# Kernel tuning notes

Measured on AMD Instinct MI355X. Metric: run time of the kernel, lower is better.

## Reference

```python
import jax, jax.numpy as jnp
import numpy as np

OUT_F, IN_F, GS = 11008, 4096, 64        # out_features, in_features, group_size
TOKENS = 4096
G = OUT_F * IN_F // GS                    # number of quantization groups = 704512


def setup_inputs() -> dict:
    key = jax.random.key(0)
    k1, k2, k3, k4, k5 = jax.random.split(key, 5)
    x = jax.random.normal(k1, (TOKENS, IN_F), dtype=jnp.float32)
    # packed 4-bit weights: two 4-bit values per byte (high nibble = first half rows)
    W_q = jax.random.randint(k2, (GS // 2, G), 0, 256, dtype=jnp.int32)
    # per-group dequant params: scale = 1/s (small positive), zero in [0, 15]
    scale = jax.random.uniform(k3, (1, G), dtype=jnp.float32, minval=1e-3, maxval=1e-2)
    zero = jax.random.uniform(k4, (1, G), dtype=jnp.float32, minval=0.0, maxval=15.0)
    bias = jax.random.normal(k5, (OUT_F,), dtype=jnp.float32) * 0.01
    return {"x": x, "W_q": W_q, "scale": scale, "zero": zero, "bias": bias}


def _dequantize(W_q, scale, zero):
    # BitPack.unpack_4bit_u8: first half of rows from high nibble, second half from low nibble
    hi = ((W_q >> 4) & 0xF).astype(jnp.float32)   # [GS//2, G]
    lo = (W_q & 0xF).astype(jnp.float32)          # [GS//2, G]
    W_r = jnp.concatenate([hi, lo], axis=0)       # [GS, G]
    # (W_r - zero) * scale, then reshape back to the original weight shape
    return ((W_r - zero) * scale).reshape(OUT_F, IN_F)


def reference(x, W_q, scale, zero, bias):
    # HQQMatmulNoCacheDeq.forward: out = x @ dequantize().T + bias
    W = _dequantize(W_q, scale, zero)             # [OUT_F, IN_F]
    return x @ W.T + bias                         # [TOKENS, OUT_F]
```

## Files before the change

kernel.cpp:

```cpp
#include <hip/hip_runtime.h>

#define TOK  4096
#define INF  4096
#define OUTF 11008
#define NG   704512
#define QD   172

typedef __bf16 bf16x8 __attribute__((ext_vector_type(8)));
typedef float  floatx4 __attribute__((ext_vector_type(4)));

__device__ inline void glds16(const __bf16* g, __bf16* l) {
  __builtin_amdgcn_global_load_lds(
      (const __attribute__((address_space(1))) void*)g,
      (__attribute__((address_space(3))) void*)l,
      16, 0, 0);
}

__global__ __launch_bounds__(256) void convert_x_kernel(
    const float* __restrict__ x, __bf16* __restrict__ Xb) {
  size_t i = ((size_t)blockIdx.x * 256 + threadIdx.x) * 8;
  float4 a = *(const float4*)(x + i);
  float4 b = *(const float4*)(x + i + 4);
  bf16x8 o;
  o[0] = (__bf16)a.x; o[1] = (__bf16)a.y; o[2] = (__bf16)a.z; o[3] = (__bf16)a.w;
  o[4] = (__bf16)b.x; o[5] = (__bf16)b.y; o[6] = (__bf16)b.z; o[7] = (__bf16)b.w;
  *(bf16x8*)(Xb + i) = o;
}

__global__ __launch_bounds__(256) void dequant_w_kernel(
    const int* __restrict__ Wq, const float* __restrict__ sc,
    const float* __restrict__ zp, __bf16* __restrict__ Wb) {
  const int b = blockIdx.x;
  const int r = b / QD;
  const int q = b - r * QD;
  const int*   wrow = Wq + (size_t)r * NG + (size_t)q * INF;
  const float* srow = sc + (size_t)q * INF;
  const float* zrow = zp + (size_t)q * INF;
  __bf16* hrow = Wb + (size_t)(r * QD + q) * INF;
  __bf16* lrow = Wb + (size_t)((r + 32) * QD + q) * INF;
#pragma unroll
  for (int it = 0; it < 2; ++it) {
    const int k = ((int)threadIdx.x + it * 256) * 8;
    int4   w0 = *(const int4*)(wrow + k);
    int4   w1 = *(const int4*)(wrow + k + 4);
    float4 s0 = *(const float4*)(srow + k);
    float4 s1 = *(const float4*)(srow + k + 4);
    float4 z0 = *(const float4*)(zrow + k);
    float4 z1 = *(const float4*)(zrow + k + 4);
    bf16x8 hi, lo;
    hi[0] = (__bf16)(((float)((w0.x >> 4) & 0xF) - z0.x) * s0.x);
    hi[1] = (__bf16)(((float)((w0.y >> 4) & 0xF) - z0.y) * s0.y);
    hi[2] = (__bf16)(((float)((w0.z >> 4) & 0xF) - z0.z) * s0.z);
    hi[3] = (__bf16)(((float)((w0.w >> 4) & 0xF) - z0.w) * s0.w);
    hi[4] = (__bf16)(((float)((w1.x >> 4) & 0xF) - z1.x) * s1.x);
    hi[5] = (__bf16)(((float)((w1.y >> 4) & 0xF) - z1.y) * s1.y);
    hi[6] = (__bf16)(((float)((w1.z >> 4) & 0xF) - z1.z) * s1.z);
    hi[7] = (__bf16)(((float)((w1.w >> 4) & 0xF) - z1.w) * s1.w);
    lo[0] = (__bf16)(((float)(w0.x & 0xF) - z0.x) * s0.x);
    lo[1] = (__bf16)(((float)(w0.y & 0xF) - z0.y) * s0.y);
    lo[2] = (__bf16)(((float)(w0.z & 0xF) - z0.z) * s0.z);
    lo[3] = (__bf16)(((float)(w0.w & 0xF) - z0.w) * s0.w);
    lo[4] = (__bf16)(((float)(w1.x & 0xF) - z1.x) * s1.x);
    lo[5] = (__bf16)(((float)(w1.y & 0xF) - z1.y) * s1.y);
    lo[6] = (__bf16)(((float)(w1.z & 0xF) - z1.z) * s1.z);
    lo[7] = (__bf16)(((float)(w1.w & 0xF) - z1.w) * s1.w);
    *(bf16x8*)(hrow + k) = hi;
    *(bf16x8*)(lrow + k) = lo;
  }
}

__global__ __launch_bounds__(256) void gemm_bt(
    const __bf16* __restrict__ Xb, const __bf16* __restrict__ Wb,
    const float* __restrict__ bias, float* __restrict__ out) {
  __shared__ __align__(16) __bf16 At[128 * 64];
  __shared__ __align__(16) __bf16 Bt[128 * 64];

  const int tid  = threadIdx.x;
  const int wave = tid >> 6;
  const int lane = tid & 63;
  const int m0 = blockIdx.y << 7;
  const int n0 = blockIdx.x << 7;

  const int wm = (wave >> 1) << 6;
  const int wn = (wave & 1) << 6;

  const __bf16* gA[4];
  const __bf16* gB[4];
  __bf16 *lA[4], *lB[4];
#pragma unroll
  for (int i = 0; i < 4; ++i) {
    const int c   = ((wave << 2) + i) * 64 + lane;
    const int row = c >> 3;
    const int j   = (c & 7) ^ (row & 7);
    gA[i] = Xb + (size_t)(m0 + row) * INF + (j << 3);
    gB[i] = Wb + (size_t)(n0 + row) * INF + (j << 3);
    lA[i] = &At[((wave << 2) + i) << 9];
    lB[i] = &Bt[((wave << 2) + i) << 9];
  }

  floatx4 acc[4][4];
  const floatx4 z4 = {0.f, 0.f, 0.f, 0.f};
#pragma unroll
  for (int mi = 0; mi < 4; ++mi)
#pragma unroll
    for (int ni = 0; ni < 4; ++ni) acc[mi][ni] = z4;

  const int fr   = lane & 15;
  const int quad = lane >> 4;

  for (int k0 = 0; k0 < INF; k0 += 64) {
    __syncthreads();
#pragma unroll
    for (int i = 0; i < 4; ++i) glds16(gA[i] + k0, lA[i]);
#pragma unroll
    for (int i = 0; i < 4; ++i) glds16(gB[i] + k0, lB[i]);
    __syncthreads();
#pragma unroll
    for (int kk = 0; kk < 2; ++kk) {
      const int j  = (kk << 2) + quad;
      const int jx = (j ^ (fr & 7)) << 3;
      bf16x8 af[4], bf[4];
#pragma unroll
      for (int mi = 0; mi < 4; ++mi)
        af[mi] = *(const bf16x8*)(At + ((wm + (mi << 4) + fr) << 6) + jx);
#pragma unroll
      for (int ni = 0; ni < 4; ++ni)
        bf[ni] = *(const bf16x8*)(Bt + ((wn + (ni << 4) + fr) << 6) + jx);
#pragma unroll
      for (int mi = 0; mi < 4; ++mi)
#pragma unroll
        for (int ni = 0; ni < 4; ++ni)
          acc[mi][ni] = __builtin_amdgcn_mfma_f32_16x16x32_bf16(
              af[mi], bf[ni], acc[mi][ni], 0, 0, 0);
    }
  }

#pragma unroll
  for (int ni = 0; ni < 4; ++ni) {
    const int n = n0 + wn + (ni << 4) + fr;
    const float bv = bias[n];
#pragma unroll
    for (int mi = 0; mi < 4; ++mi) {
      const int mbase = m0 + wm + (mi << 4) + (quad << 2);
#pragma unroll
      for (int j = 0; j < 4; ++j) {
        out[(size_t)(mbase + j) * OUTF + n] = acc[mi][ni][j] + bv;
      }
    }
  }
}

extern "C" void kernel_launch(void* const* d_in, const int* in_sizes, int n_in,
                              void* d_out, int out_size, void* d_ws, size_t ws_size,
                              hipStream_t stream) {
  const float* x  = (const float*)d_in[0];
  const int*   Wq = (const int*)d_in[1];
  const float* sc = (const float*)d_in[2];
  const float* zp = (const float*)d_in[3];
  const float* bs = (const float*)d_in[4];
  float* out = (float*)d_out;

  __bf16* Xb = (__bf16*)d_ws;
  __bf16* Wb = Xb + (size_t)TOK * INF;

  convert_x_kernel<<<dim3((TOK * INF) / (256 * 8)), dim3(256), 0, stream>>>(x, Xb);
  dequant_w_kernel<<<dim3(32 * QD), dim3(256), 0, stream>>>(Wq, sc, zp, Wb);
  gemm_bt<<<dim3(OUTF / 128, TOK / 128), dim3(256), 0, stream>>>(Xb, Wb, bs, out);
}
```

Before: 782.3 us.

## Enlarge GEMM tiles to 256x256 with double-buffered LDS and swizzled block order

```diff
diff --git a/kernel.cpp b/kernel.cpp
--- a/kernel.cpp
+++ b/kernel.cpp
@@ -69,82 +69,124 @@
   }
 }
 
-__global__ __launch_bounds__(256) void gemm_bt(
+
+#define MM_QUARTER(A_, JX, MOFF)                                              \
+    _Pragma("unroll") for (int mi = 0; mi < 4; ++mi)                          \
+      afr[mi] = *(const bf16x8*)((A_) + aoff + ((mi + (MOFF)) << 10) + (JX)); \
+    __builtin_amdgcn_s_setprio(1);                                            \
+    _Pragma("unroll") for (int mi = 0; mi < 4; ++mi)                          \
+      _Pragma("unroll") for (int ni = 0; ni < 4; ++ni)                        \
+        acc[mi + (MOFF)][ni] = __builtin_amdgcn_mfma_f32_16x16x32_bf16(       \
+            afr[mi], bfr[ni], acc[mi + (MOFF)][ni], 0, 0, 0);                 \
+    __builtin_amdgcn_s_setprio(0);
+
+#define KTILE_COMPUTE(BUF)                                                    \
+  { const __bf16* A_ = &As[BUF][0];                                           \
+    const __bf16* B_ = &Bs[BUF][0];                                           \
+    bf16x8 afr[4], bfr[4];                                                    \
+    _Pragma("unroll") for (int ni = 0; ni < 4; ++ni)                          \
+      bfr[ni] = *(const bf16x8*)(B_ + boff + (ni << 10) + jx0);               \
+    MM_QUARTER(A_, jx0, 0)                                                    \
+    MM_QUARTER(A_, jx0, 4)                                                    \
+    _Pragma("unroll") for (int ni = 0; ni < 4; ++ni)                          \
+      bfr[ni] = *(const bf16x8*)(B_ + boff + (ni << 10) + jx1);               \
+    MM_QUARTER(A_, jx1, 0)                                                    \
+    MM_QUARTER(A_, jx1, 4)                                                    \
+  }
+
+#define KTILE_SYNC(BUF, DO_STAGE, KOFF2, VMC)                                 \
+    asm volatile("s_waitcnt lgkmcnt(0)" ::: "memory");                        \
+    __builtin_amdgcn_s_barrier();                                             \
+    asm volatile("" ::: "memory");                                            \
+    if (DO_STAGE) {                                                           \
+      _Pragma("unroll") for (int r = 0; r < 4; ++r)                           \
+        glds16(gA[r] + (KOFF2), (BUF) ? lA1[r] : lA0[r]);                     \
+      _Pragma("unroll") for (int r = 0; r < 4; ++r)                           \
+        glds16(gB[r] + (KOFF2), (BUF) ? lB1[r] : lB0[r]);                     \
+    }                                                                         \
+    if ((VMC) == 8) { asm volatile("s_waitcnt vmcnt(8)" ::: "memory"); }      \
+    else            { asm volatile("s_waitcnt vmcnt(0)" ::: "memory"); }      \
+    __builtin_amdgcn_s_barrier();                                             \
+    asm volatile("" ::: "memory");
+
+__global__ __launch_bounds__(512, 2) void gemm_bt(
     const __bf16* __restrict__ Xb, const __bf16* __restrict__ Wb,
     const float* __restrict__ bias, float* __restrict__ out) {
-  __shared__ __align__(16) __bf16 At[128 * 64];
-  __shared__ __align__(16) __bf16 Bt[128 * 64];
+  __shared__ __align__(16) __bf16 As[2][256 * 64];
+  __shared__ __align__(16) __bf16 Bs[2][256 * 64];
 
   const int tid  = threadIdx.x;
   const int wave = tid >> 6;
   const int lane = tid & 63;
-  const int m0 = blockIdx.y << 7;
-  const int n0 = blockIdx.x << 7;
-
-  const int wm = (wave >> 1) << 6;
-  const int wn = (wave & 1) << 6;
-
-  const __bf16* gA[4];
-  const __bf16* gB[4];
-  __bf16 *lA[4], *lB[4];
-#pragma unroll
-  for (int i = 0; i < 4; ++i) {
-    const int c   = ((wave << 2) + i) * 64 + lane;
+
+  const int orig = blockIdx.x;
+  const int swz  = (orig & 7) * 86 + (orig >> 3);
+  const int bn   = swz % 43;
+  const int bm   = swz / 43;
+  const int m0   = bm << 8;
+  const int n0   = bn << 8;
+
+  const int wm = (wave >> 2) << 7;
+  const int wn = (wave & 3) << 6;
+
+  const __bf16* gA[4]; const __bf16* gB[4];
+  __bf16 *lA0[4], *lB0[4], *lA1[4], *lB1[4];
+#pragma unroll
+  for (int r = 0; r < 4; ++r) {
+    const int c   = (r << 9) + tid;
     const int row = c >> 3;
     const int j   = (c & 7) ^ (row & 7);
-    gA[i] = Xb + (size_t)(m0 + row) * INF + (j << 3);
-    gB[i] = Wb + (size_t)(n0 + row) * INF + (j << 3);
-    lA[i] = &At[((wave << 2) + i) << 9];
-    lB[i] = &Bt[((wave << 2) + i) << 9];
-  }
-
-  floatx4 acc[4][4];
+    gA[r] = Xb + (size_t)(m0 + row) * INF + (j << 3);
+    gB[r] = Wb + (size_t)(n0 + row) * INF + (j << 3);
+    const int lbase = ((r << 9) + (wave << 6)) << 3;
+    lA0[r] = &As[0][lbase]; lA1[r] = &As[1][lbase];
+    lB0[r] = &Bs[0][lbase]; lB1[r] = &Bs[1][lbase];
+  }
+
+#pragma unroll
+  for (int r = 0; r < 4; ++r) glds16(gA[r], lA0[r]);
+#pragma unroll
+  for (int r = 0; r < 4; ++r) glds16(gB[r], lB0[r]);
+#pragma unroll
+  for (int r = 0; r < 4; ++r) glds16(gA[r] + 64, lA1[r]);
+#pragma unroll
+  for (int r = 0; r < 4; ++r) glds16(gB[r] + 64, lB1[r]);
+
+  floatx4 acc[8][4];
   const floatx4 z4 = {0.f, 0.f, 0.f, 0.f};
 #pragma unroll
-  for (int mi = 0; mi < 4; ++mi)
+  for (int mi = 0; mi < 8; ++mi)
 #pragma unroll
     for (int ni = 0; ni < 4; ++ni) acc[mi][ni] = z4;
 
   const int fr   = lane & 15;
   const int quad = lane >> 4;
-
-  for (int k0 = 0; k0 < INF; k0 += 64) {
-    __syncthreads();
-#pragma unroll
-    for (int i = 0; i < 4; ++i) glds16(gA[i] + k0, lA[i]);
-#pragma unroll
-    for (int i = 0; i < 4; ++i) glds16(gB[i] + k0, lB[i]);
-    __syncthreads();
-#pragma unroll
-    for (int kk = 0; kk < 2; ++kk) {
-      const int j  = (kk << 2) + quad;
-      const int jx = (j ^ (fr & 7)) << 3;
-      bf16x8 af[4], bf[4];
-#pragma unroll
-      for (int mi = 0; mi < 4; ++mi)
-        af[mi] = *(const bf16x8*)(At + ((wm + (mi << 4) + fr) << 6) + jx);
-#pragma unroll
-      for (int ni = 0; ni < 4; ++ni)
-        bf[ni] = *(const bf16x8*)(Bt + ((wn + (ni << 4) + fr) << 6) + jx);
-#pragma unroll
-      for (int mi = 0; mi < 4; ++mi)
-#pragma unroll
-        for (int ni = 0; ni < 4; ++ni)
-          acc[mi][ni] = __builtin_amdgcn_mfma_f32_16x16x32_bf16(
-              af[mi], bf[ni], acc[mi][ni], 0, 0, 0);
-    }
-  }
+  const int jx0  = ((0 * 4 + quad) ^ (fr & 7)) << 3;
+  const int jx1  = ((1 * 4 + quad) ^ (fr & 7)) << 3;
+  const int aoff = (wm + fr) << 6;
+  const int boff = (wn + fr) << 6;
+
+  asm volatile("s_waitcnt vmcnt(8)" ::: "memory");
+  __builtin_amdgcn_s_barrier();
+  asm volatile("" ::: "memory");
+
+  for (int t = 0; t < 62; t += 2) {
+    KTILE_COMPUTE(0) KTILE_SYNC(0, 1, ((t + 2) << 6), 8)
+    KTILE_COMPUTE(1) KTILE_SYNC(1, 1, ((t + 3) << 6), 8)
+  }
+  KTILE_COMPUTE(0) KTILE_SYNC(0, 0, 0, 0)
+  KTILE_COMPUTE(1)
 
 #pragma unroll
   for (int ni = 0; ni < 4; ++ni) {
     const int n = n0 + wn + (ni << 4) + fr;
     const float bv = bias[n];
 #pragma unroll
-    for (int mi = 0; mi < 4; ++mi) {
-      const int mbase = m0 + wm + (mi << 4) + (quad << 2);
+    for (int mi = 0; mi < 8; ++mi) {
+      const int mb = m0 + wm + (mi << 4) + (quad << 2);
 #pragma unroll
       for (int j = 0; j < 4; ++j) {
-        out[(size_t)(mbase + j) * OUTF + n] = acc[mi][ni][j] + bv;
+        out[(size_t)(mb + j) * OUTF + n] = acc[mi][ni][j] + bv;
       }
     }
   }
@@ -165,5 +207,5 @@
 
   convert_x_kernel<<<dim3((TOK * INF) / (256 * 8)), dim3(256), 0, stream>>>(x, Xb);
   dequant_w_kernel<<<dim3(32 * QD), dim3(256), 0, stream>>>(Wq, sc, zp, Wb);
-  gemm_bt<<<dim3(OUTF / 128, TOK / 128), dim3(256), 0, stream>>>(Xb, Wb, bs, out);
-}
+  gemm_bt<<<dim3(OUTF / 256 * (TOK / 256)), dim3(512), 0, stream>>>(Xb, Wb, bs, out);
+}
```

Result: faster. 688.0 us (-12.1%).
